# Optimization experiments

Hardware: AMD Instinct MI355X
Metric: run time of the kernel (lower is better)

Reference implementation:

```python
import jax, jax.numpy as jnp
import numpy as np

BS, NA, NE_, NL = 128, 3, 3, 3
NALL = NA - 1                 # n_allies
ENT = NA + NE_ + NL           # 9 entities
EM1 = ENT - 1                 # 8
HID = 64                      # hidden_dim
HEAD = 4
HIN = 9                       # hyper input dim
HYP = 64                      # hyper hidden dim
NRBF, RUB = 3, 10.0
EPS = 1e-7


def _lin_init(k, fan_in, fan_out):
    k1, k2 = jax.random.split(k)
    lim = 1.0 / np.sqrt(fan_in)
    w = jax.random.uniform(k1, (fan_in, fan_out), minval=-lim, maxval=lim, dtype=jnp.float32)
    b = jax.random.uniform(k2, (fan_out,), minval=-lim, maxval=lim, dtype=jnp.float32)
    return w, b


def setup_inputs():
    key = jax.random.key(0)
    ks = jax.random.split(key, 12)
    d = {}
    obs_dim = 4 + 2 * (NL + NALL + NE_) + 2 * (NALL + NE_)  # 30
    d["inputs"] = jax.random.normal(ks[0], (BS * NA, obs_dim), dtype=jnp.float32)
    d["hidden_state"] = jnp.zeros((1, HID), dtype=jnp.float32)
    d["actions"] = jax.random.normal(ks[1], (BS * NA, 2), dtype=jnp.float32)
    out_dim = (HIN + 1) * HID * HEAD  # 2560
    d["hA1_w"], d["hA1_b"] = _lin_init(ks[2], HIN, HYP)
    d["hA2_w"], d["hA2_b"] = _lin_init(ks[3], HYP, out_dim)
    d["hE1_w"], d["hE1_b"] = _lin_init(ks[4], HIN, HYP)
    d["hE2_w"], d["hE2_b"] = _lin_init(ks[5], HYP, out_dim)
    d["hL1_w"], d["hL1_b"] = _lin_init(ks[6], HIN, HYP)
    d["hL2_w"], d["hL2_b"] = _lin_init(ks[7], HYP, out_dim)
    d["merger_w"] = jnp.ones((1, HEAD, HID), dtype=jnp.float32)
    d["fc1_w"], d["fc1_b"] = _lin_init(ks[8], HID + 3, HID)
    d["fc2_w"], d["fc2_b"] = _lin_init(ks[9], HID, 1)
    return d


def _pair_out(feat, w1, b1, w2, b2):
    # hypernetwork: Linear(9,64) -> LeakyReLU -> Linear(64, (9+1)*64*4)
    h = jax.nn.leaky_relu(feat @ w1 + b1, negative_slope=0.01)
    out = h @ w2 + b2                               # (bs,NA,EM1,EM1,2560)
    nw = HIN * HID * HEAD
    w = out[..., :nw].reshape(feat.shape[:-1] + (HIN, HID * HEAD))
    b = out[..., nw:]
    y = jnp.einsum('...k,...kd->...d', feat, w) + b  # tiny 1x9 @ 9x256 per pair
    return y.reshape(feat.shape[:-1] + (HEAD, HID))


def _forward(inputs, actions, hA1_w, hA1_b, hA2_w, hA2_b, hE1_w, hE1_b, hE2_w, hE2_b,
             hL1_w, hL1_b, hL2_w, hL2_b, merger_w, fc1_w, fc1_b, fc2_w, fc2_b):
    bs = inputs.shape[0] // NA
    ob = inputs
    own = ob[:, :4].reshape(bs, NA, 4)
    i = 4
    lm_pos = ob[:, i:i + NL * 2].reshape(bs, NA, NL, 2); i += NL * 2
    ally_pos = ob[:, i:i + NALL * 2].reshape(bs, NA, NALL, 2); i += NALL * 2
    enemy_pos = ob[:, i:i + NE_ * 2].reshape(bs, NA, NE_, 2); i += NE_ * 2
    entity_pos = jnp.concatenate([ally_pos, enemy_pos, lm_pos], axis=-2)  # (bs,NA,EM1,2)
    ally_vel = ob[:, i:i + NALL * 2].reshape(bs, NA, NALL, 2); i += NALL * 2
    enemy_vel = ob[:, i:i + NE_ * 2].reshape(bs, NA, NE_, 2)
    lm_vel = jnp.zeros_like(lm_pos) - own[:, :, None, :2]
    entity_vel = jnp.concatenate([ally_vel, enemy_vel, lm_vel], axis=-2)  # (bs,NA,EM1,2)
    # rel_vel[b,a,j,i] = vel[i] - vel[j]
    rel_vel = entity_vel[:, :, None, :, :] - entity_vel[:, :, :, None, :]
    vel_norm = jnp.sqrt((entity_vel ** 2).sum(-1))
    sin_a = entity_vel[..., 1] / (vel_norm + EPS)
    cos_a = entity_vel[..., 0] / (vel_norm + EPS)
    act = actions.reshape(bs, NA, 2)
    act_norm = jnp.sqrt((act ** 2).sum(-1))        # (bs,NA)
    sin_b = act[..., 1] / (act_norm + EPS)
    cos_b = act[..., 0] / (act_norm + EPS)
    dist = jnp.sqrt((entity_pos ** 2).sum(-1))     # (bs,NA,EM1)
    sin_t = entity_pos[..., 1] / (dist + EPS)
    cos_t = entity_pos[..., 0] / (dist + EPS)
    # pair angles: A,C vary over last axis (i), B over second-to-last (j)
    sA, cA = sin_t[:, :, None, :], cos_t[:, :, None, :]
    sB, cB = sin_t[:, :, :, None], cos_t[:, :, :, None]
    sC, cC = sin_a[:, :, None, :], cos_a[:, :, None, :]
    angle_info = jnp.stack([sA * cB - cA * sB, cA * cB + sA * sB,
                            sC * cB - cC * sB, cC * cB + sC * sB], axis=-1)
    angle_info = jnp.broadcast_to(angle_info, (bs, NA, EM1, EM1, 4))
    sD, cD = sin_b[:, :, None], cos_b[:, :, None]
    act_angle = jnp.stack([sD * cos_t - cD * sin_t, cD * cos_t + sD * sin_t], axis=-1)  # (bs,NA,EM1,2)
    # gaussian RBF (schnet-style smearing, num_rbf=3, rbound_upper=10)
    offset = jnp.linspace(0.0, RUB, NRBF)
    coeff = -0.5 / (offset[1] - offset[0]) ** 2
    rbf = jnp.exp(coeff * (dist[..., None] - offset) ** 2)  # (bs,NA,EM1,NRBF)
    feat_dist = jnp.broadcast_to(rbf[:, :, None, :, :], (bs, NA, EM1, EM1, NRBF))
    feat = jnp.concatenate([feat_dist, angle_info, rel_vel], axis=-1)  # (bs,NA,EM1,EM1,9)
    ally_out = _pair_out(feat, hA1_w, hA1_b, hA2_w, hA2_b)
    enemy_out = _pair_out(feat, hE1_w, hE1_b, hE2_w, hE2_b)
    lm_out = _pair_out(feat, hL1_w, hL1_b, hL2_w, hL2_b)
    # type-based selection over the source-entity axis (dim 3), then sum-aggregate
    m = jnp.concatenate([ally_out[:, :, :, :NALL],
                         enemy_out[:, :, :, NALL:NALL + NE_],
                         lm_out[:, :, :, NALL + NE_:]], axis=3)
    m_sum = m.sum(axis=3)                               # (bs,NA,EM1,HEAD,HID)
    mw = jax.nn.softmax(merger_w, axis=1)               # (1,HEAD,HID)
    m_jki = (mw * m_sum).sum(axis=-2)                   # (bs,NA,EM1,HID)
    an = jnp.broadcast_to(act_norm[:, :, None], (bs, NA, EM1))[..., None]
    final = jnp.concatenate([m_jki, an, act_angle], axis=-1)  # (bs,NA,EM1,HID+3)
    x = jax.nn.relu(final)
    x = jax.nn.relu(x @ fc1_w + fc1_b)
    q = (x @ fc2_w + fc2_b).mean(axis=-2).reshape(-1, 1)  # (bs*NA,1)
    return q, x


def reference(inputs, hidden_state, actions, hA1_w, hA1_b, hA2_w, hA2_b,
              hE1_w, hE1_b, hE2_w, hE2_b, hL1_w, hL1_b, hL2_w, hL2_b,
              merger_w, fc1_w, fc1_b, fc2_w, fc2_b):
    q, x = _forward(inputs, actions, hA1_w, hA1_b, hA2_w, hA2_b,
                    hE1_w, hE1_b, hE2_w, hE2_b, hL1_w, hL1_b, hL2_w, hL2_b,
                    merger_w, fc1_w, fc1_b, fc2_w, fc2_b)
    return q, x
```

## Files before the change

kernel.cpp:

```cpp
#include <hip/hip_runtime.h>
#include <math.h>

#define EPS 1e-7f
#define ROWP 656
#define NETS 3
#define NROW_TOT (NETS*ROWP)
#define G4 (ROWP/4)
#define GPW (G4/4)
#define PERNET4 (G4*64)

__global__ __launch_bounds__(256) void prep_w2r(
    const float* __restrict__ W2A, const float* __restrict__ b2A,
    const float* __restrict__ W2E, const float* __restrict__ b2E,
    const float* __restrict__ W2L, const float* __restrict__ b2L,
    const float* __restrict__ merger, float* __restrict__ W2r)
{
    int idx = blockIdx.x * 256 + threadIdx.x;
    if (idx >= NETS * PERNET4) return;
    int net = idx / PERNET4;
    int rem = idx - net * PERNET4;
    int g4  = rem >> 6;
    int hid = rem & 63;

    float m0 = merger[hid], m1 = merger[64+hid], m2 = merger[128+hid], m3 = merger[192+hid];
    float mx = fmaxf(fmaxf(m0, m1), fmaxf(m2, m3));
    float e0 = expf(m0-mx), e1 = expf(m1-mx), e2 = expf(m2-mx), e3 = expf(m3-mx);
    float inv = 1.0f / (e0+e1+e2+e3);
    float w0 = e0*inv, w1 = e1*inv, w2 = e2*inv, w3 = e3*inv;

    const float* W2 = (net==0) ? W2A : ((net==1) ? W2E : W2L);
    const float* b2 = (net==0) ? b2A : ((net==1) ? b2E : b2L);

    float4 v;
    float* vp = &v.x;
    #pragma unroll
    for (int r = 0; r < 4; ++r) {
        int row = g4*4 + r;
        float val = 0.0f;
        if (row < 650) {
            const float* src;
            int kk;
            if (row < 640) { kk = row >> 6; int h = row & 63; src = W2 + h*2560; }
            else           { kk = row - 640;                  src = b2; }
            int col = (kk < 9) ? kk*256 : 2304;
            val = w0*src[col+hid] + w1*src[col+64+hid] + w2*src[col+128+hid] + w3*src[col+192+hid];
        }
        vp[r] = val;
    }
    ((float4*)W2r)[idx] = v;
}

__global__ __launch_bounds__(256, 2) void agent_kernel(
    const float* __restrict__ inputs, const float* __restrict__ actions,
    const float* __restrict__ W1A, const float* __restrict__ b1A,
    const float* __restrict__ W1E, const float* __restrict__ b1E,
    const float* __restrict__ W1L, const float* __restrict__ b1L,
    const float* __restrict__ W2r,
    const float* __restrict__ fc1w, const float* __restrict__ fc1b,
    const float* __restrict__ fc2w, const float* __restrict__ fc2b,
    float* __restrict__ out_q, float* __restrict__ out_x)
{
    __shared__ float sOb[32];
    __shared__ float sSt[8], sCt[8], sSa[8], sCa[8], sVx[8], sVy[8];
    __shared__ float sRbf[8][3];
    __shared__ float sAct[3];
    __shared__ float sF[64][10];
    __shared__ __align__(16) float sU[8 * NROW_TOT];
    __shared__ float sZp[4][8][64];
    __shared__ float sZ[8][64];
    __shared__ float sRed[4];

    const int tid   = threadIdx.x;
    const int agent = blockIdx.x;

    if (tid < 30) sOb[tid] = inputs[agent*30 + tid];
    if (tid == 30) sOb[30] = actions[agent*2 + 0];
    if (tid == 31) sOb[31] = actions[agent*2 + 1];
    __syncthreads();

    if (tid < 8) {
        int e = tid;
        float px, py, vx, vy;
        if (e < 2)      {           px = sOb[10+2*e]; py = sOb[11+2*e]; vx = sOb[20+2*e]; vy = sOb[21+2*e]; }
        else if (e < 5) { int t=e-2; px = sOb[14+2*t]; py = sOb[15+2*t]; vx = sOb[24+2*t]; vy = sOb[25+2*t]; }
        else            { int t=e-5; px = sOb[4+2*t];  py = sOb[5+2*t];  vx = -sOb[0];     vy = -sOb[1]; }
        float d  = sqrtf(px*px + py*py);
        sSt[e] = py / (d + EPS);
        sCt[e] = px / (d + EPS);
        float vn = sqrtf(vx*vx + vy*vy);
        sSa[e] = vy / (vn + EPS);
        sCa[e] = vx / (vn + EPS);
        sVx[e] = vx; sVy[e] = vy;
        sRbf[e][0] = expf(-0.02f * d * d);
        float d5  = d - 5.0f;  sRbf[e][1] = expf(-0.02f * d5  * d5);
        float d10 = d - 10.0f; sRbf[e][2] = expf(-0.02f * d10 * d10);
    }
    if (tid == 8) {
        float ax = sOb[30], ay = sOb[31];
        float an = sqrtf(ax*ax + ay*ay);
        sAct[0] = an;
        sAct[1] = ay / (an + EPS);
        sAct[2] = ax / (an + EPS);
    }
    __syncthreads();

    if (tid < 64) {
        int p = tid, j = p >> 3, k = p & 7;
        sF[p][0] = sRbf[k][0];
        sF[p][1] = sRbf[k][1];
        sF[p][2] = sRbf[k][2];
        sF[p][3] = sSt[k]*sCt[j] - sCt[k]*sSt[j];
        sF[p][4] = sCt[k]*sCt[j] + sSt[k]*sSt[j];
        sF[p][5] = sSa[k]*sCt[j] - sCa[k]*sSt[j];
        sF[p][6] = sCa[k]*sCt[j] + sSa[k]*sSt[j];
        sF[p][7] = sVx[k] - sVx[j];
        sF[p][8] = sVy[k] - sVy[j];
        sF[p][9] = 1.0f;
    }
    __syncthreads();

    for (int e = tid; e < 1920; e += 256) {
        if (e < 1536) {
            int j = e / 192, rem = e - j*192;
            int net = rem >> 6, h = rem & 63;
            int ks = (net==0) ? 0 : ((net==1) ? 2 : 5);
            int kn = (net==0) ? 2 : 3;
            const float* W1 = (net==0) ? W1A : ((net==1) ? W1E : W1L);
            const float* b1 = (net==0) ? b1A : ((net==1) ? b1E : b1L);
            float v[10];
            #pragma unroll
            for (int kk = 0; kk < 10; ++kk) v[kk] = 0.0f;
            for (int q = 0; q < kn; ++q) {
                int p = j*8 + ks + q;
                float acc = b1[h];
                #pragma unroll
                for (int kk = 0; kk < 9; ++kk) acc = fmaf(sF[p][kk], W1[kk*64 + h], acc);
                float H = (acc > 0.0f) ? acc : 0.01f*acc;
                #pragma unroll
                for (int kk = 0; kk < 10; ++kk) v[kk] = fmaf(H, sF[p][kk], v[kk]);
            }
            float* dst = sU + j*NROW_TOT + net*ROWP + h;
            #pragma unroll
            for (int kk = 0; kk < 10; ++kk) dst[kk*64] = v[kk];
        } else if (e < 1776) {
            int t = e - 1536;
            int j = t / 30, rem = t - j*30;
            int net = rem / 10, kk = rem - net*10;
            int ks = (net==0) ? 0 : ((net==1) ? 2 : 5);
            int kn = (net==0) ? 2 : 3;
            float v = 0.0f;
            for (int q = 0; q < kn; ++q) v += sF[j*8 + ks + q][kk];
            sU[j*NROW_TOT + net*ROWP + 640 + kk] = v;
        } else {
            int t = e - 1776;
            int j = t / 18, rem = t - j*18;
            int net = rem / 6, r = rem - net*6;
            sU[j*NROW_TOT + net*ROWP + 650 + r] = 0.0f;
        }
    }
    __syncthreads();

    {
        const int lane = tid & 63, w = tid >> 6;
        const int q = lane >> 4, hh = lane & 15;
        float acc[8][4];
        #pragma unroll
        for (int j = 0; j < 8; ++j)
            #pragma unroll
            for (int k = 0; k < 4; ++k) acc[j][k] = 0.0f;

        const float4* Wp = (const float4*)W2r;
        const int base = w * GPW;
        for (int net = 0; net < NETS; ++net) {
            const float4* Wn = Wp + net*PERNET4;
            const float*  Ub = sU + net*ROWP;
            #pragma unroll 2
            for (int u = 0; u < 10; ++u) {
                int g = base + u*4 + q;
                const float4* wb = Wn + g*64 + hh;
                float4 wk0 = wb[0], wk1 = wb[16], wk2 = wb[32], wk3 = wb[48];
                float4 uj[8];
                #pragma unroll
                for (int j = 0; j < 8; ++j) uj[j] = *(const float4*)(Ub + j*NROW_TOT + g*4);
                #pragma unroll
                for (int j = 0; j < 8; ++j) {
                    float4 uu = uj[j];
                    acc[j][0] = fmaf(uu.x,wk0.x, fmaf(uu.y,wk0.y, fmaf(uu.z,wk0.z, fmaf(uu.w,wk0.w, acc[j][0]))));
                    acc[j][1] = fmaf(uu.x,wk1.x, fmaf(uu.y,wk1.y, fmaf(uu.z,wk1.z, fmaf(uu.w,wk1.w, acc[j][1]))));
                    acc[j][2] = fmaf(uu.x,wk2.x, fmaf(uu.y,wk2.y, fmaf(uu.z,wk2.z, fmaf(uu.w,wk2.w, acc[j][2]))));
                    acc[j][3] = fmaf(uu.x,wk3.x, fmaf(uu.y,wk3.y, fmaf(uu.z,wk3.z, fmaf(uu.w,wk3.w, acc[j][3]))));
                }
            }
            if (q == 0) {
                int g = base + 40;
                const float4* wb = Wn + g*64 + hh;
                float4 wk0 = wb[0], wk1 = wb[16], wk2 = wb[32], wk3 = wb[48];
                #pragma unroll
                for (int j = 0; j < 8; ++j) {
                    float4 uu = *(const float4*)(Ub + j*NROW_TOT + g*4);
                    acc[j][0] = fmaf(uu.x,wk0.x, fmaf(uu.y,wk0.y, fmaf(uu.z,wk0.z, fmaf(uu.w,wk0.w, acc[j][0]))));
                    acc[j][1] = fmaf(uu.x,wk1.x, fmaf(uu.y,wk1.y, fmaf(uu.z,wk1.z, fmaf(uu.w,wk1.w, acc[j][1]))));
                    acc[j][2] = fmaf(uu.x,wk2.x, fmaf(uu.y,wk2.y, fmaf(uu.z,wk2.z, fmaf(uu.w,wk2.w, acc[j][2]))));
                    acc[j][3] = fmaf(uu.x,wk3.x, fmaf(uu.y,wk3.y, fmaf(uu.z,wk3.z, fmaf(uu.w,wk3.w, acc[j][3]))));
                }
            }
        }
        #pragma unroll
        for (int j = 0; j < 8; ++j) {
            #pragma unroll
            for (int k = 0; k < 4; ++k) {
                float v = acc[j][k];
                v += __shfl_xor(v, 16);
                v += __shfl_xor(v, 32);
                if (q == 0) sZp[w][j][k*16 + hh] = v;
            }
        }
    }
    __syncthreads();
    for (int o = tid; o < 512; o += 256) {
        int j = o >> 6, c = o & 63;
        float z = sZp[0][j][c] + sZp[1][j][c] + sZp[2][j][c] + sZp[3][j][c];
        sZ[j][c] = (z > 0.0f) ? z : 0.0f;
    }
    __syncthreads();

    {
        float an  = sAct[0], sb = sAct[1], cb = sAct[2];
        float anr = (an > 0.0f) ? an : 0.0f;
        float myq = 0.0f;
        #pragma unroll
        for (int i = 0; i < 2; ++i) {
            int o = i*256 + tid;
            int j = o >> 6, c = o & 63;
            float acc = fc1b[c];
            #pragma unroll 8
            for (int d = 0; d < 64; ++d)
                acc = fmaf(sZ[j][d], fc1w[d*64 + c], acc);
            float aa0 = sb*sCt[j] - cb*sSt[j];
            float aa1 = cb*sCt[j] + sb*sSt[j];
            aa0 = (aa0 > 0.0f) ? aa0 : 0.0f;
            aa1 = (aa1 > 0.0f) ? aa1 : 0.0f;
            acc = fmaf(anr, fc1w[64*64 + c], acc);
            acc = fmaf(aa0, fc1w[65*64 + c], acc);
            acc = fmaf(aa1, fc1w[66*64 + c], acc);
            float x1 = (acc > 0.0f) ? acc : 0.0f;
            out_x[(agent*8 + j)*64 + c] = x1;
            myq = fmaf(x1, fc2w[c], myq);
        }
        for (int off = 32; off; off >>= 1) myq += __shfl_down(myq, off);
        int lane = tid & 63, w = tid >> 6;
        if (lane == 0) sRed[w] = myq;
        __syncthreads();
        if (tid == 0) out_q[agent] = (sRed[0] + sRed[1] + sRed[2] + sRed[3]) * 0.125f + fc2b[0];
    }
}

extern "C" void kernel_launch(void* const* d_in, const int* in_sizes, int n_in,
                              void* d_out, int out_size, void* d_ws, size_t ws_size,
                              hipStream_t stream) {
    const float* inputs  = (const float*)d_in[0];
    const float* actions = (const float*)d_in[2];
    const float* hA1_w = (const float*)d_in[3];  const float* hA1_b = (const float*)d_in[4];
    const float* hA2_w = (const float*)d_in[5];  const float* hA2_b = (const float*)d_in[6];
    const float* hE1_w = (const float*)d_in[7];  const float* hE1_b = (const float*)d_in[8];
    const float* hE2_w = (const float*)d_in[9];  const float* hE2_b = (const float*)d_in[10];
    const float* hL1_w = (const float*)d_in[11]; const float* hL1_b = (const float*)d_in[12];
    const float* hL2_w = (const float*)d_in[13]; const float* hL2_b = (const float*)d_in[14];
    const float* merger = (const float*)d_in[15];
    const float* fc1w = (const float*)d_in[16];  const float* fc1b = (const float*)d_in[17];
    const float* fc2w = (const float*)d_in[18];  const float* fc2b = (const float*)d_in[19];

    float* W2r = (float*)d_ws;
    float* q   = (float*)d_out;
    float* x   = q + 384;

    int total4 = NETS * PERNET4;
    prep_w2r<<<(total4 + 255)/256, 256, 0, stream>>>(hA2_w, hA2_b, hE2_w, hE2_b,
                                                     hL2_w, hL2_b, merger, W2r);
    agent_kernel<<<384, 256, 0, stream>>>(inputs, actions,
                                          hA1_w, hA1_b, hE1_w, hE1_b, hL1_w, hL1_b,
                                          W2r, fc1w, fc1b, fc2w, fc2b, q, x);
}
```

Baseline: 121.0 us.

## Split hypernetwork contraction into two half-blocks per agent with separate epilogue kernel

Splits the per-agent reduction over the 10 hypernetwork input rows into two halves, so 768 blocks each handle five rows with a smaller shared-memory tile and higher occupancy (launch bounds raised to 3). Partial sums go to a workspace buffer, and a new epilogue kernel combines them and runs fc1/fc2. The inner loop is software-pipelined with register double-buffering of weight and U loads. This adds a third launch, a global round trip for partials, and recomputation of the first-layer hidden activations in both halves.

```diff
diff --git a/kernel.cpp b/kernel.cpp
--- a/kernel.cpp
+++ b/kernel.cpp
@@ -2,12 +2,12 @@
 #include <math.h>
 
 #define EPS 1e-7f
-#define ROWP 656
 #define NETS 3
-#define NROW_TOT (NETS*ROWP)
-#define G4 (ROWP/4)
-#define GPW (G4/4)
-#define PERNET4 (G4*64)
+#define HROWP 384
+#define HG    (HROWP/4)
+#define GPW   (HG/4)
+#define JSTRIDE (NETS*HROWP)
+#define W2R_F4_TOT (2*NETS*HG*64)
 
 __global__ __launch_bounds__(256) void prep_w2r(
     const float* __restrict__ W2A, const float* __restrict__ b2A,
@@ -16,11 +16,13 @@
     const float* __restrict__ merger, float* __restrict__ W2r)
 {
     int idx = blockIdx.x * 256 + threadIdx.x;
-    if (idx >= NETS * PERNET4) return;
-    int net = idx / PERNET4;
-    int rem = idx - net * PERNET4;
-    int g4  = rem >> 6;
-    int hid = rem & 63;
+    if (idx >= W2R_F4_TOT) return;
+    int half = idx / (NETS*HG*64);
+    int rem  = idx - half * (NETS*HG*64);
+    int net  = rem / (HG*64);
+    rem     -= net * (HG*64);
+    int g4   = rem >> 6;
+    int hid  = rem & 63;
 
     float m0 = merger[hid], m1 = merger[64+hid], m2 = merger[128+hid], m3 = merger[192+hid];
     float mx = fmaxf(fmaxf(m0, m1), fmaxf(m2, m3));
@@ -37,11 +39,11 @@
     for (int r = 0; r < 4; ++r) {
         int row = g4*4 + r;
         float val = 0.0f;
-        if (row < 650) {
+        if (row < 325) {
             const float* src;
             int kk;
-            if (row < 640) { kk = row >> 6; int h = row & 63; src = W2 + h*2560; }
-            else           { kk = row - 640;                  src = b2; }
+            if (row < 320) { kk = half*5 + (row >> 6); int h = row & 63; src = W2 + h*2560; }
+            else           { kk = half*5 + (row - 320);                  src = b2; }
             int col = (kk < 9) ? kk*256 : 2304;
             val = w0*src[col+hid] + w1*src[col+64+hid] + w2*src[col+128+hid] + w3*src[col+192+hid];
         }
@@ -50,28 +52,23 @@
     ((float4*)W2r)[idx] = v;
 }
 
-__global__ __launch_bounds__(256, 2) void agent_kernel(
+__global__ __launch_bounds__(256, 3) void half_kernel(
     const float* __restrict__ inputs, const float* __restrict__ actions,
     const float* __restrict__ W1A, const float* __restrict__ b1A,
     const float* __restrict__ W1E, const float* __restrict__ b1E,
     const float* __restrict__ W1L, const float* __restrict__ b1L,
-    const float* __restrict__ W2r,
-    const float* __restrict__ fc1w, const float* __restrict__ fc1b,
-    const float* __restrict__ fc2w, const float* __restrict__ fc2b,
-    float* __restrict__ out_q, float* __restrict__ out_x)
+    const float* __restrict__ W2r, float* __restrict__ Zpart)
 {
     __shared__ float sOb[32];
     __shared__ float sSt[8], sCt[8], sSa[8], sCa[8], sVx[8], sVy[8];
     __shared__ float sRbf[8][3];
-    __shared__ float sAct[3];
     __shared__ float sF[64][10];
-    __shared__ __align__(16) float sU[8 * NROW_TOT];
+    __shared__ __align__(16) float sU[8 * JSTRIDE];
     __shared__ float sZp[4][8][64];
-    __shared__ float sZ[8][64];
-    __shared__ float sRed[4];
 
     const int tid   = threadIdx.x;
-    const int agent = blockIdx.x;
+    const int agent = blockIdx.x >> 1;
+    const int half  = blockIdx.x & 1;
 
     if (tid < 30) sOb[tid] = inputs[agent*30 + tid];
     if (tid == 30) sOb[30] = actions[agent*2 + 0];
@@ -95,13 +92,6 @@
         float d5  = d - 5.0f;  sRbf[e][1] = expf(-0.02f * d5  * d5);
         float d10 = d - 10.0f; sRbf[e][2] = expf(-0.02f * d10 * d10);
     }
-    if (tid == 8) {
-        float ax = sOb[30], ay = sOb[31];
-        float an = sqrtf(ax*ax + ay*ay);
-        sAct[0] = an;
-        sAct[1] = ay / (an + EPS);
-        sAct[2] = ax / (an + EPS);
-    }
     __syncthreads();
 
     if (tid < 64) {
@@ -119,91 +109,87 @@
     }
     __syncthreads();
 
-    for (int e = tid; e < 1920; e += 256) {
-        if (e < 1536) {
-            int j = e / 192, rem = e - j*192;
-            int net = rem >> 6, h = rem & 63;
+    for (int e = tid; e < 1536; e += 256) {
+        int j = e / 192, rem = e - j*192;
+        int net = rem >> 6, r = rem & 63;
+        float v = 0.0f;
+        if (r < 5) {
+            int kk = half*5 + r;
             int ks = (net==0) ? 0 : ((net==1) ? 2 : 5);
             int kn = (net==0) ? 2 : 3;
-            const float* W1 = (net==0) ? W1A : ((net==1) ? W1E : W1L);
-            const float* b1 = (net==0) ? b1A : ((net==1) ? b1E : b1L);
-            float v[10];
-            #pragma unroll
-            for (int kk = 0; kk < 10; ++kk) v[kk] = 0.0f;
-            for (int q = 0; q < kn; ++q) {
-                int p = j*8 + ks + q;
-                float acc = b1[h];
-                #pragma unroll
-                for (int kk = 0; kk < 9; ++kk) acc = fmaf(sF[p][kk], W1[kk*64 + h], acc);
-                float H = (acc > 0.0f) ? acc : 0.01f*acc;
-                #pragma unroll
-                for (int kk = 0; kk < 10; ++kk) v[kk] = fmaf(H, sF[p][kk], v[kk]);
-            }
-            float* dst = sU + j*NROW_TOT + net*ROWP + h;
-            #pragma unroll
-            for (int kk = 0; kk < 10; ++kk) dst[kk*64] = v[kk];
-        } else if (e < 1776) {
-            int t = e - 1536;
-            int j = t / 30, rem = t - j*30;
-            int net = rem / 10, kk = rem - net*10;
-            int ks = (net==0) ? 0 : ((net==1) ? 2 : 5);
-            int kn = (net==0) ? 2 : 3;
-            float v = 0.0f;
             for (int q = 0; q < kn; ++q) v += sF[j*8 + ks + q][kk];
-            sU[j*NROW_TOT + net*ROWP + 640 + kk] = v;
-        } else {
-            int t = e - 1776;
-            int j = t / 18, rem = t - j*18;
-            int net = rem / 6, r = rem - net*6;
-            sU[j*NROW_TOT + net*ROWP + 650 + r] = 0.0f;
-        }
+        }
+        sU[(j*NETS + net)*HROWP + 320 + r] = v;
+    }
+    for (int e = tid; e < 1536; e += 256) {
+        int j = e / 192, rem = e - j*192;
+        int net = rem >> 6, h = rem & 63;
+        int ks = (net==0) ? 0 : ((net==1) ? 2 : 5);
+        int kn = (net==0) ? 2 : 3;
+        const float* W1 = (net==0) ? W1A : ((net==1) ? W1E : W1L);
+        const float* b1 = (net==0) ? b1A : ((net==1) ? b1E : b1L);
+        float v[5];
+        #pragma unroll
+        for (int c = 0; c < 5; ++c) v[c] = 0.0f;
+        for (int q = 0; q < kn; ++q) {
+            int p = j*8 + ks + q;
+            float acc = b1[h];
+            #pragma unroll
+            for (int kk = 0; kk < 9; ++kk) acc = fmaf(sF[p][kk], W1[kk*64 + h], acc);
+            float H = (acc > 0.0f) ? acc : 0.01f*acc;
+            #pragma unroll
+            for (int c = 0; c < 5; ++c) v[c] = fmaf(H, sF[p][half*5 + c], v[c]);
+        }
+        float* dst = sU + (j*NETS + net)*HROWP + h;
+        #pragma unroll
+        for (int c = 0; c < 5; ++c) dst[c*64] = v[c];
     }
     __syncthreads();
 
     {
         const int lane = tid & 63, w = tid >> 6;
         const int q = lane >> 4, hh = lane & 15;
+        const int base = w * GPW;
         float acc[8][4];
         #pragma unroll
         for (int j = 0; j < 8; ++j)
             #pragma unroll
             for (int k = 0; k < 4; ++k) acc[j][k] = 0.0f;
 
-        const float4* Wp = (const float4*)W2r;
-        const int base = w * GPW;
-        for (int net = 0; net < NETS; ++net) {
-            const float4* Wn = Wp + net*PERNET4;
-            const float*  Ub = sU + net*ROWP;
-            #pragma unroll 2
-            for (int u = 0; u < 10; ++u) {
-                int g = base + u*4 + q;
-                const float4* wb = Wn + g*64 + hh;
-                float4 wk0 = wb[0], wk1 = wb[16], wk2 = wb[32], wk3 = wb[48];
-                float4 uj[8];
+        const float4* Wbase = (const float4*)W2r + (size_t)half * (NETS*HG*64);
+
+        float4 wk0, wk1, wk2, wk3, cu[8];
+        {
+            int g = base + q;
+            const float4* wb = Wbase + g*64 + hh;
+            wk0 = wb[0]; wk1 = wb[16]; wk2 = wb[32]; wk3 = wb[48];
+            const float* Ub = sU + g*4;
+            #pragma unroll
+            for (int j = 0; j < 8; ++j) cu[j] = *(const float4*)(Ub + j*JSTRIDE);
+        }
+        for (int it = 0; it < 18; ++it) {
+            float4 nk0, nk1, nk2, nk3, nu[8];
+            if (it < 17) {
+                int nit = it + 1;
+                int nnet = nit / 6, nu_ = nit - nnet*6;
+                int ng = base + nu_*4 + q;
+                const float4* wb = Wbase + (nnet*HG + ng)*64 + hh;
+                nk0 = wb[0]; nk1 = wb[16]; nk2 = wb[32]; nk3 = wb[48];
+                const float* Ub = sU + nnet*HROWP + ng*4;
                 #pragma unroll
-                for (int j = 0; j < 8; ++j) uj[j] = *(const float4*)(Ub + j*NROW_TOT + g*4);
-                #pragma unroll
-                for (int j = 0; j < 8; ++j) {
-                    float4 uu = uj[j];
-                    acc[j][0] = fmaf(uu.x,wk0.x, fmaf(uu.y,wk0.y, fmaf(uu.z,wk0.z, fmaf(uu.w,wk0.w, acc[j][0]))));
-                    acc[j][1] = fmaf(uu.x,wk1.x, fmaf(uu.y,wk1.y, fmaf(uu.z,wk1.z, fmaf(uu.w,wk1.w, acc[j][1]))));
-                    acc[j][2] = fmaf(uu.x,wk2.x, fmaf(uu.y,wk2.y, fmaf(uu.z,wk2.z, fmaf(uu.w,wk2.w, acc[j][2]))));
-                    acc[j][3] = fmaf(uu.x,wk3.x, fmaf(uu.y,wk3.y, fmaf(uu.z,wk3.z, fmaf(uu.w,wk3.w, acc[j][3]))));
-                }
+                for (int j = 0; j < 8; ++j) nu[j] = *(const float4*)(Ub + j*JSTRIDE);
             }
-            if (q == 0) {
-                int g = base + 40;
-                const float4* wb = Wn + g*64 + hh;
-                float4 wk0 = wb[0], wk1 = wb[16], wk2 = wb[32], wk3 = wb[48];
-                #pragma unroll
-                for (int j = 0; j < 8; ++j) {
-                    float4 uu = *(const float4*)(Ub + j*NROW_TOT + g*4);
-                    acc[j][0] = fmaf(uu.x,wk0.x, fmaf(uu.y,wk0.y, fmaf(uu.z,wk0.z, fmaf(uu.w,wk0.w, acc[j][0]))));
-                    acc[j][1] = fmaf(uu.x,wk1.x, fmaf(uu.y,wk1.y, fmaf(uu.z,wk1.z, fmaf(uu.w,wk1.w, acc[j][1]))));
-                    acc[j][2] = fmaf(uu.x,wk2.x, fmaf(uu.y,wk2.y, fmaf(uu.z,wk2.z, fmaf(uu.w,wk2.w, acc[j][2]))));
-                    acc[j][3] = fmaf(uu.x,wk3.x, fmaf(uu.y,wk3.y, fmaf(uu.z,wk3.z, fmaf(uu.w,wk3.w, acc[j][3]))));
-                }
+            #pragma unroll
+            for (int j = 0; j < 8; ++j) {
+                float4 uu = cu[j];
+                acc[j][0] = fmaf(uu.x,wk0.x, fmaf(uu.y,wk0.y, fmaf(uu.z,wk0.z, fmaf(uu.w,wk0.w, acc[j][0]))));
+                acc[j][1] = fmaf(uu.x,wk1.x, fmaf(uu.y,wk1.y, fmaf(uu.z,wk1.z, fmaf(uu.w,wk1.w, acc[j][1]))));
+                acc[j][2] = fmaf(uu.x,wk2.x, fmaf(uu.y,wk2.y, fmaf(uu.z,wk2.z, fmaf(uu.w,wk2.w, acc[j][2]))));
+                acc[j][3] = fmaf(uu.x,wk3.x, fmaf(uu.y,wk3.y, fmaf(uu.z,wk3.z, fmaf(uu.w,wk3.w, acc[j][3]))));
             }
+            wk0 = nk0; wk1 = nk1; wk2 = nk2; wk3 = nk3;
+            #pragma unroll
+            for (int j = 0; j < 8; ++j) cu[j] = nu[j];
         }
         #pragma unroll
         for (int j = 0; j < 8; ++j) {
@@ -217,42 +203,87 @@
         }
     }
     __syncthreads();
+    {
+        float* dst = Zpart + (size_t)agent*1024 + half*512;
+        for (int o = tid; o < 512; o += 256) {
+            int j = o >> 6, c = o & 63;
+            dst[o] = sZp[0][j][c] + sZp[1][j][c] + sZp[2][j][c] + sZp[3][j][c];
+        }
+    }
+}
+
+__global__ __launch_bounds__(256) void epilogue_kernel(
+    const float* __restrict__ inputs, const float* __restrict__ actions,
+    const float* __restrict__ Zpart,
+    const float* __restrict__ fc1w, const float* __restrict__ fc1b,
+    const float* __restrict__ fc2w, const float* __restrict__ fc2b,
+    float* __restrict__ out_q, float* __restrict__ out_x)
+{
+    __shared__ float sOb[32];
+    __shared__ float sSt[8], sCt[8];
+    __shared__ float sAct[3];
+    __shared__ float sZ[8][64];
+    __shared__ float sRed[4];
+
+    const int tid   = threadIdx.x;
+    const int agent = blockIdx.x;
+
+    if (tid < 30) sOb[tid] = inputs[agent*30 + tid];
+    if (tid == 30) sOb[30] = actions[agent*2 + 0];
+    if (tid == 31) sOb[31] = actions[agent*2 + 1];
+    __syncthreads();
+
+    if (tid < 8) {
+        int e = tid;
+        float px, py;
+        if (e < 2)      {           px = sOb[10+2*e]; py = sOb[11+2*e]; }
+        else if (e < 5) { int t=e-2; px = sOb[14+2*t]; py = sOb[15+2*t]; }
+        else            { int t=e-5; px = sOb[4+2*t];  py = sOb[5+2*t]; }
+        float d = sqrtf(px*px + py*py);
+        sSt[e] = py / (d + EPS);
+        sCt[e] = px / (d + EPS);
+    }
+    if (tid == 8) {
+        float ax = sOb[30], ay = sOb[31];
+        float an = sqrtf(ax*ax + ay*ay);
+        sAct[0] = an;
+        sAct[1] = ay / (an + EPS);
+        sAct[2] = ax / (an + EPS);
+    }
+    const float* Zp = Zpart + (size_t)agent*1024;
     for (int o = tid; o < 512; o += 256) {
+        float z = Zp[o] + Zp[512 + o];
+        ((float*)sZ)[o] = (z > 0.0f) ? z : 0.0f;
+    }
+    __syncthreads();
+
+    float an  = sAct[0], sb = sAct[1], cb = sAct[2];
+    float anr = (an > 0.0f) ? an : 0.0f;
+    float myq = 0.0f;
+    #pragma unroll
+    for (int i = 0; i < 2; ++i) {
+        int o = i*256 + tid;
         int j = o >> 6, c = o & 63;
-        float z = sZp[0][j][c] + sZp[1][j][c] + sZp[2][j][c] + sZp[3][j][c];
-        sZ[j][c] = (z > 0.0f) ? z : 0.0f;
-    }
-    __syncthreads();
-
-    {
-        float an  = sAct[0], sb = sAct[1], cb = sAct[2];
-        float anr = (an > 0.0f) ? an : 0.0f;
-        float myq = 0.0f;
-        #pragma unroll
-        for (int i = 0; i < 2; ++i) {
-            int o = i*256 + tid;
-            int j = o >> 6, c = o & 63;
-            float acc = fc1b[c];
-            #pragma unroll 8
-            for (int d = 0; d < 64; ++d)
-                acc = fmaf(sZ[j][d], fc1w[d*64 + c], acc);
-            float aa0 = sb*sCt[j] - cb*sSt[j];
-            float aa1 = cb*sCt[j] + sb*sSt[j];
-            aa0 = (aa0 > 0.0f) ? aa0 : 0.0f;
-            aa1 = (aa1 > 0.0f) ? aa1 : 0.0f;
-            acc = fmaf(anr, fc1w[64*64 + c], acc);
-            acc = fmaf(aa0, fc1w[65*64 + c], acc);
-            acc = fmaf(aa1, fc1w[66*64 + c], acc);
-            float x1 = (acc > 0.0f) ? acc : 0.0f;
-            out_x[(agent*8 + j)*64 + c] = x1;
-            myq = fmaf(x1, fc2w[c], myq);
-        }
-        for (int off = 32; off; off >>= 1) myq += __shfl_down(myq, off);
-        int lane = tid & 63, w = tid >> 6;
-        if (lane == 0) sRed[w] = myq;
-        __syncthreads();
-        if (tid == 0) out_q[agent] = (sRed[0] + sRed[1] + sRed[2] + sRed[3]) * 0.125f + fc2b[0];
-    }
+        float acc = fc1b[c];
+        #pragma unroll 8
+        for (int d = 0; d < 64; ++d)
+            acc = fmaf(sZ[j][d], fc1w[d*64 + c], acc);
+        float aa0 = sb*sCt[j] - cb*sSt[j];
+        float aa1 = cb*sCt[j] + sb*sSt[j];
+        aa0 = (aa0 > 0.0f) ? aa0 : 0.0f;
+        aa1 = (aa1 > 0.0f) ? aa1 : 0.0f;
+        acc = fmaf(anr, fc1w[64*64 + c], acc);
+        acc = fmaf(aa0, fc1w[65*64 + c], acc);
+        acc = fmaf(aa1, fc1w[66*64 + c], acc);
+        float x1 = (acc > 0.0f) ? acc : 0.0f;
+        out_x[(agent*8 + j)*64 + c] = x1;
+        myq = fmaf(x1, fc2w[c], myq);
+    }
+    for (int off = 32; off; off >>= 1) myq += __shfl_down(myq, off);
+    int lane = tid & 63, w = tid >> 6;
+    if (lane == 0) sRed[w] = myq;
+    __syncthreads();
+    if (tid == 0) out_q[agent] = (sRed[0] + sRed[1] + sRed[2] + sRed[3]) * 0.125f + fc2b[0];
 }
 
 extern "C" void kernel_launch(void* const* d_in, const int* in_sizes, int n_in,
@@ -270,14 +301,15 @@
     const float* fc1w = (const float*)d_in[16];  const float* fc1b = (const float*)d_in[17];
     const float* fc2w = (const float*)d_in[18];  const float* fc2b = (const float*)d_in[19];
 
-    float* W2r = (float*)d_ws;
-    float* q   = (float*)d_out;
-    float* x   = q + 384;
-
-    int total4 = NETS * PERNET4;
-    prep_w2r<<<(total4 + 255)/256, 256, 0, stream>>>(hA2_w, hA2_b, hE2_w, hE2_b,
-                                                     hL2_w, hL2_b, merger, W2r);
-    agent_kernel<<<384, 256, 0, stream>>>(inputs, actions,
-                                          hA1_w, hA1_b, hE1_w, hE1_b, hL1_w, hL1_b,
-                                          W2r, fc1w, fc1b, fc2w, fc2b, q, x);
+    float* W2r   = (float*)d_ws;
+    float* Zpart = (float*)((char*)d_ws + 589824);
+    float* q     = (float*)d_out;
+    float* x     = q + 384;
+
+    prep_w2r<<<(W2R_F4_TOT + 255)/256, 256, 0, stream>>>(
+        hA2_w, hA2_b, hE2_w, hE2_b, hL2_w, hL2_b, merger, W2r);
+    half_kernel<<<768, 256, 0, stream>>>(
+        inputs, actions, hA1_w, hA1_b, hE1_w, hE1_b, hL1_w, hL1_b, W2r, Zpart);
+    epilogue_kernel<<<384, 256, 0, stream>>>(
+        inputs, actions, Zpart, fc1w, fc1b, fc2w, fc2b, q, x);
 }
```

New measurement: 122.1 us. About the same (+0.9%).
